# Kernel optimization log

Hardware: AMD Instinct MI355X
Metric: run time of the kernel (lower is better)

## Reference

```python
import jax, jax.numpy as jnp
import numpy as np

EPS = 1e-8  # torch.nn.CosineSimilarity default eps


def setup_inputs() -> dict:
    key = jax.random.key(0)
    k1, k2, k3 = jax.random.split(key, 3)
    B, T, D, L = 16, 256, 512, 32
    v1 = jax.random.normal(k1, (B, T, D), dtype=jnp.float32)
    v1_mask = jnp.ones((B, T), dtype=jnp.float32)
    v2 = jax.random.normal(k2, (B, D), dtype=jnp.float32)
    w = jax.random.normal(k3, (L, D), dtype=jnp.float32)
    return {"v1": v1, "v1_mask": v1_mask, "v2": v2, "w": w}


def reference(v1, v1_mask, v2, w):
    # v1: [B,T,D], v1_mask: [B,T], v2: [B,D], w: [L,D]
    # Original math: cos over D of (w * v1) and (w * v2), per perspective l.
    # Fused: (w_l*a)\cdot(w_l*b) = sum_d w[l,d]^2 a[d] b[d]; likewise for norms.
    v1m = v1 * v1_mask[:, :, None]              # [B,T,D]
    w2 = w * w                                   # [L,D]
    num = jnp.einsum('btd,ld,bd->btl', v1m, w2, v2)          # [B,T,L]
    n1 = jnp.sqrt(jnp.einsum('btd,ld->btl', v1m * v1m, w2))  # [B,T,L]
    n2 = jnp.sqrt(jnp.einsum('bd,ld->bl', v2 * v2, w2))      # [B,L]
    denom = jnp.maximum(n1 * n2[:, None, :], EPS)
    return num / denom                           # [B,T,L]
```

## Files before the change

kernel.cpp:

```cpp
#include <hip/hip_runtime.h>
#include <cstddef>

#define EPSV 1e-8f

__device__ __forceinline__ float rdlane(float x, int s) {
    return __int_as_float(__builtin_amdgcn_readlane(__float_as_int(x), s));
}

#define GLD16(gp, lp) \
    __builtin_amdgcn_global_load_lds((const __attribute__((address_space(1))) void*)(gp), \
                                     (__attribute__((address_space(3))) void*)(lp), 16, 0, 0)

__global__ __launch_bounds__(256, 2) void fullmatch_kernel(
    const float* __restrict__ v1,
    const float* __restrict__ v1_mask,
    const float* __restrict__ v2,
    const float* __restrict__ w,
    float* __restrict__ out)
{
    const int tid  = threadIdx.x;
    const int lane = tid & 63;
    const int wv   = tid >> 6;
    const int lp2  = wv & 1;
    const int dh   = wv >> 1;
    const int dh16 = __builtin_amdgcn_readfirstlane(dh) * 16;

    const int bid  = blockIdx.x;
    const int tile = bid & 63;
    const int lpg  = bid >> 6;
    const int b    = tile >> 2;
    const int t0   = (tile & 3) * 64;
    const int p    = lpg * 2 + lp2;
    const int t    = t0 + lane;

    __shared__ float v1s[2][64][128];
    __shared__ float cmb[4][64][4];

    const size_t v1base = (size_t)(b * 256 + t0) * 512;

    #pragma unroll
    for (int j = 0; j < 8; ++j) {
        const int r0 = wv * 16 + j * 2;
        const int r  = r0 + (lane >> 5);
        const int c4 = (lane & 31) ^ (r & 31);
        GLD16(v1 + v1base + (size_t)r * 512 + c4 * 4, &v1s[0][r0][0]);
    }

    float4 w2A[2], w2B[2], hA[2], hB[2];
    float n2pA = 0.f, n2pB = 0.f;
    {
        const float* __restrict__ v2b = v2 + (size_t)b * 512;
        const float* __restrict__ wAp = w + (size_t)p * 512;
        const float* __restrict__ wBp = w + (size_t)(p + 16) * 512;
        #pragma unroll
        for (int q = 0; q < 2; ++q) {
            const int k4 = q * 64 + lane;
            const float4 wa = *(const float4*)(wAp + k4 * 4);
            const float4 wb = *(const float4*)(wBp + k4 * 4);
            const float4 vv = *(const float4*)(v2b + k4 * 4);
            float4 sa, sb, ha, hb;
            sa.x = wa.x*wa.x; sa.y = wa.y*wa.y; sa.z = wa.z*wa.z; sa.w = wa.w*wa.w;
            sb.x = wb.x*wb.x; sb.y = wb.y*wb.y; sb.z = wb.z*wb.z; sb.w = wb.w*wb.w;
            ha.x = sa.x*vv.x; ha.y = sa.y*vv.y; ha.z = sa.z*vv.z; ha.w = sa.w*vv.w;
            hb.x = sb.x*vv.x; hb.y = sb.y*vv.y; hb.z = sb.z*vv.z; hb.w = sb.w*vv.w;
            w2A[q] = sa; w2B[q] = sb; hA[q] = ha; hB[q] = hb;
            n2pA += ha.x*vv.x + ha.y*vv.y + ha.z*vv.z + ha.w*vv.w;
            n2pB += hb.x*vv.x + hb.y*vv.y + hb.z*vv.z + hb.w*vv.w;
        }
    }
    #pragma unroll
    for (int m = 32; m >= 1; m >>= 1) {
        n2pA += __shfl_xor(n2pA, m, 64);
        n2pB += __shfl_xor(n2pB, m, 64);
    }

    float accNA = 0.f, accNB = 0.f, accDA = 0.f, accDB = 0.f;
    const int lm = lane & 31;

    #pragma unroll
    for (int c = 0; c < 4; ++c) {
        __syncthreads();
        if (c < 3) {
            #pragma unroll
            for (int j = 0; j < 8; ++j) {
                const int r0 = wv * 16 + j * 2;
                const int r  = r0 + (lane >> 5);
                const int c4 = (lane & 31) ^ (r & 31);
                GLD16(v1 + v1base + (size_t)r * 512 + (c + 1) * 128 + c4 * 4,
                      &v1s[(c + 1) & 1][r0][0]);
            }
        }
        const float* __restrict__ row = &v1s[c & 1][lane][0];
        #pragma unroll
        for (int j = 0; j < 16; ++j) {
            const int s  = dh16 + j;
            const float4 a = *(const float4*)(row + ((s ^ lm) << 2));
            const int li = ((c & 1) << 5) + s;
            const int q  = c >> 1;

            const float wax = rdlane(w2A[q].x, li);
            const float way = rdlane(w2A[q].y, li);
            const float waz = rdlane(w2A[q].z, li);
            const float waw = rdlane(w2A[q].w, li);
            const float wbx = rdlane(w2B[q].x, li);
            const float wby = rdlane(w2B[q].y, li);
            const float wbz = rdlane(w2B[q].z, li);
            const float wbw = rdlane(w2B[q].w, li);
            const float hax = rdlane(hA[q].x, li);
            const float hay = rdlane(hA[q].y, li);
            const float haz = rdlane(hA[q].z, li);
            const float haw = rdlane(hA[q].w, li);
            const float hbx = rdlane(hB[q].x, li);
            const float hby = rdlane(hB[q].y, li);
            const float hbz = rdlane(hB[q].z, li);
            const float hbw = rdlane(hB[q].w, li);

            const float x2 = a.x * a.x, y2 = a.y * a.y;
            const float z2 = a.z * a.z, q2 = a.w * a.w;

            accNA = fmaf(a.x, hax, accNA);
            accNA = fmaf(a.y, hay, accNA);
            accNA = fmaf(a.z, haz, accNA);
            accNA = fmaf(a.w, haw, accNA);
            accNB = fmaf(a.x, hbx, accNB);
            accNB = fmaf(a.y, hby, accNB);
            accNB = fmaf(a.z, hbz, accNB);
            accNB = fmaf(a.w, hbw, accNB);
            accDA = fmaf(x2, wax, accDA);
            accDA = fmaf(y2, way, accDA);
            accDA = fmaf(z2, waz, accDA);
            accDA = fmaf(q2, waw, accDA);
            accDB = fmaf(x2, wbx, accDB);
            accDB = fmaf(y2, wby, accDB);
            accDB = fmaf(z2, wbz, accDB);
            accDB = fmaf(q2, wbw, accDB);
        }
    }

    cmb[wv][lane][0] = accNA;
    cmb[wv][lane][1] = accNB;
    cmb[wv][lane][2] = accDA;
    cmb[wv][lane][3] = accDB;
    __syncthreads();

    if (wv < 2) {
        const float4 o = *(const float4*)(&cmb[wv + 2][lane][0]);
        const float nA = accNA + o.x;
        const float nB = accNB + o.y;
        const float dA = accDA + o.z;
        const float dB = accDB + o.w;

        const float mk  = v1_mask[b * 256 + t];
        const float amk = fabsf(mk);
        const float n2vA = sqrtf(n2pA);
        const float n2vB = sqrtf(n2pB);
        const float denA = fmaxf(sqrtf(dA) * amk * n2vA, EPSV);
        const float denB = fmaxf(sqrtf(dB) * amk * n2vB, EPSV);
        const size_t oix = (size_t)(b * 256 + t) * 32;
        out[oix + p]      = (nA * mk) / denA;
        out[oix + p + 16] = (nB * mk) / denB;
    }
}

extern "C" void kernel_launch(void* const* d_in, const int* in_sizes, int n_in,
                              void* d_out, int out_size, void* d_ws, size_t ws_size,
                              hipStream_t stream) {
    const float* v1      = (const float*)d_in[0];
    const float* v1_mask = (const float*)d_in[1];
    const float* v2      = (const float*)d_in[2];
    const float* w       = (const float*)d_in[3];
    float* out           = (float*)d_out;

    fullmatch_kernel<<<dim3(512), dim3(256), 0, stream>>>(v1, v1_mask, v2, w, out);
}
```

Measured before the change: 19.66 us.

## Split D across four waves with per-wave LDS staging and no block barriers

```diff
diff --git a/kernel.cpp b/kernel.cpp
--- a/kernel.cpp
+++ b/kernel.cpp
@@ -11,7 +11,7 @@
     __builtin_amdgcn_global_load_lds((const __attribute__((address_space(1))) void*)(gp), \
                                      (__attribute__((address_space(3))) void*)(lp), 16, 0, 0)
 
-__global__ __launch_bounds__(256, 2) void fullmatch_kernel(
+__global__ __launch_bounds__(256, 4) void fullmatch_kernel(
     const float* __restrict__ v1,
     const float* __restrict__ v1_mask,
     const float* __restrict__ v2,
@@ -21,99 +21,112 @@
     const int tid  = threadIdx.x;
     const int lane = tid & 63;
     const int wv   = tid >> 6;
-    const int lp2  = wv & 1;
-    const int dh   = wv >> 1;
-    const int dh16 = __builtin_amdgcn_readfirstlane(dh) * 16;
+    const int wvu  = __builtin_amdgcn_readfirstlane(wv);
 
     const int bid  = blockIdx.x;
     const int tile = bid & 63;
     const int lpg  = bid >> 6;
     const int b    = tile >> 2;
     const int t0   = (tile & 3) * 64;
-    const int p    = lpg * 2 + lp2;
+    const int p    = lpg;
     const int t    = t0 + lane;
 
-    __shared__ float v1s[2][64][128];
+    __shared__ float buf[4][2][64][16];
     __shared__ float cmb[4][64][4];
 
-    const size_t v1base = (size_t)(b * 256 + t0) * 512;
+    const size_t rowbase = (size_t)(b * 256 + t0) * 512;
+    const int    qoff    = wvu * 128;
 
-    #pragma unroll
-    for (int j = 0; j < 8; ++j) {
-        const int r0 = wv * 16 + j * 2;
-        const int r  = r0 + (lane >> 5);
-        const int c4 = (lane & 31) ^ (r & 31);
-        GLD16(v1 + v1base + (size_t)r * 512 + c4 * 4, &v1s[0][r0][0]);
-    }
+    #define STAGE(sc, bs)                                                          \
+        do {                                                                       \
+            _Pragma("unroll")                                                      \
+            for (int i = 0; i < 4; ++i) {                                          \
+                const int r = i * 16 + (lane >> 2);                                \
+                const int m = (lane & 3) ^ ((lane >> 3) & 3);                      \
+                GLD16(v1 + rowbase + (size_t)r * 512 + qoff + (sc) * 16 + m * 4,   \
+                      &buf[wv][bs][i * 16][0]);                                    \
+            }                                                                      \
+        } while (0)
 
-    float4 w2A[2], w2B[2], hA[2], hB[2];
+    STAGE(0, 0);
+
+    float4 w2A0, w2A1, w2B0, w2B1, hA0, hA1, hB0, hB1;
     float n2pA = 0.f, n2pB = 0.f;
     {
         const float* __restrict__ v2b = v2 + (size_t)b * 512;
         const float* __restrict__ wAp = w + (size_t)p * 512;
         const float* __restrict__ wBp = w + (size_t)(p + 16) * 512;
-        #pragma unroll
-        for (int q = 0; q < 2; ++q) {
-            const int k4 = q * 64 + lane;
-            const float4 wa = *(const float4*)(wAp + k4 * 4);
-            const float4 wb = *(const float4*)(wBp + k4 * 4);
-            const float4 vv = *(const float4*)(v2b + k4 * 4);
-            float4 sa, sb, ha, hb;
-            sa.x = wa.x*wa.x; sa.y = wa.y*wa.y; sa.z = wa.z*wa.z; sa.w = wa.w*wa.w;
-            sb.x = wb.x*wb.x; sb.y = wb.y*wb.y; sb.z = wb.z*wb.z; sb.w = wb.w*wb.w;
-            ha.x = sa.x*vv.x; ha.y = sa.y*vv.y; ha.z = sa.z*vv.z; ha.w = sa.w*vv.w;
-            hb.x = sb.x*vv.x; hb.y = sb.y*vv.y; hb.z = sb.z*vv.z; hb.w = sb.w*vv.w;
-            w2A[q] = sa; w2B[q] = sb; hA[q] = ha; hB[q] = hb;
-            n2pA += ha.x*vv.x + ha.y*vv.y + ha.z*vv.z + ha.w*vv.w;
-            n2pB += hb.x*vv.x + hb.y*vv.y + hb.z*vv.z + hb.w*vv.w;
+        {
+            const float4 wa = *(const float4*)(wAp + lane * 4);
+            const float4 wb = *(const float4*)(wBp + lane * 4);
+            const float4 vv = *(const float4*)(v2b + lane * 4);
+            w2A0.x = wa.x*wa.x; w2A0.y = wa.y*wa.y; w2A0.z = wa.z*wa.z; w2A0.w = wa.w*wa.w;
+            w2B0.x = wb.x*wb.x; w2B0.y = wb.y*wb.y; w2B0.z = wb.z*wb.z; w2B0.w = wb.w*wb.w;
+            hA0.x = w2A0.x*vv.x; hA0.y = w2A0.y*vv.y; hA0.z = w2A0.z*vv.z; hA0.w = w2A0.w*vv.w;
+            hB0.x = w2B0.x*vv.x; hB0.y = w2B0.y*vv.y; hB0.z = w2B0.z*vv.z; hB0.w = w2B0.w*vv.w;
+            n2pA += hA0.x*vv.x + hA0.y*vv.y + hA0.z*vv.z + hA0.w*vv.w;
+            n2pB += hB0.x*vv.x + hB0.y*vv.y + hB0.z*vv.z + hB0.w*vv.w;
+        }
+        {
+            const float4 wa = *(const float4*)(wAp + 256 + lane * 4);
+            const float4 wb = *(const float4*)(wBp + 256 + lane * 4);
+            const float4 vv = *(const float4*)(v2b + 256 + lane * 4);
+            w2A1.x = wa.x*wa.x; w2A1.y = wa.y*wa.y; w2A1.z = wa.z*wa.z; w2A1.w = wa.w*wa.w;
+            w2B1.x = wb.x*wb.x; w2B1.y = wb.y*wb.y; w2B1.z = wb.z*wb.z; w2B1.w = wb.w*wb.w;
+            hA1.x = w2A1.x*vv.x; hA1.y = w2A1.y*vv.y; hA1.z = w2A1.z*vv.z; hA1.w = w2A1.w*vv.w;
+            hB1.x = w2B1.x*vv.x; hB1.y = w2B1.y*vv.y; hB1.z = w2B1.z*vv.z; hB1.w = w2B1.w*vv.w;
+            n2pA += hA1.x*vv.x + hA1.y*vv.y + hA1.z*vv.z + hA1.w*vv.w;
+            n2pB += hB1.x*vv.x + hB1.y*vv.y + hB1.z*vv.z + hB1.w*vv.w;
         }
     }
-    #pragma unroll
-    for (int m = 32; m >= 1; m >>= 1) {
-        n2pA += __shfl_xor(n2pA, m, 64);
-        n2pB += __shfl_xor(n2pB, m, 64);
+    if (wvu == 0) {
+        #pragma unroll
+        for (int m = 32; m >= 1; m >>= 1) {
+            n2pA += __shfl_xor(n2pA, m, 64);
+            n2pB += __shfl_xor(n2pB, m, 64);
+        }
     }
 
+    const int hi = wvu >> 1;
+    const float4 sw2A = hi ? w2A1 : w2A0;
+    const float4 sw2B = hi ? w2B1 : w2B0;
+    const float4 shA  = hi ? hA1  : hA0;
+    const float4 shB  = hi ? hB1  : hB0;
+    const int libase  = (wvu & 1) << 5;
+
     float accNA = 0.f, accNB = 0.f, accDA = 0.f, accDB = 0.f;
-    const int lm = lane & 31;
+    const int swz = (lane >> 1) & 3;
 
-    #pragma unroll
-    for (int c = 0; c < 4; ++c) {
-        __syncthreads();
-        if (c < 3) {
-            #pragma unroll
-            for (int j = 0; j < 8; ++j) {
-                const int r0 = wv * 16 + j * 2;
-                const int r  = r0 + (lane >> 5);
-                const int c4 = (lane & 31) ^ (r & 31);
-                GLD16(v1 + v1base + (size_t)r * 512 + (c + 1) * 128 + c4 * 4,
-                      &v1s[(c + 1) & 1][r0][0]);
-            }
+    #pragma unroll 2
+    for (int sc = 0; sc < 8; ++sc) {
+        if (sc < 7) {
+            STAGE(sc + 1, (sc + 1) & 1);
+            asm volatile("s_waitcnt vmcnt(4)" ::: "memory");
+        } else {
+            asm volatile("s_waitcnt vmcnt(0)" ::: "memory");
         }
-        const float* __restrict__ row = &v1s[c & 1][lane][0];
+        const float* __restrict__ rowp = &buf[wv][sc & 1][lane][0];
         #pragma unroll
-        for (int j = 0; j < 16; ++j) {
-            const int s  = dh16 + j;
-            const float4 a = *(const float4*)(row + ((s ^ lm) << 2));
-            const int li = ((c & 1) << 5) + s;
-            const int q  = c >> 1;
+        for (int j = 0; j < 4; ++j) {
+            const float4 a = *(const float4*)(rowp + ((j ^ swz) << 2));
+            const int li = libase + sc * 4 + j;
 
-            const float wax = rdlane(w2A[q].x, li);
-            const float way = rdlane(w2A[q].y, li);
-            const float waz = rdlane(w2A[q].z, li);
-            const float waw = rdlane(w2A[q].w, li);
-            const float wbx = rdlane(w2B[q].x, li);
-            const float wby = rdlane(w2B[q].y, li);
-            const float wbz = rdlane(w2B[q].z, li);
-            const float wbw = rdlane(w2B[q].w, li);
-            const float hax = rdlane(hA[q].x, li);
-            const float hay = rdlane(hA[q].y, li);
-            const float haz = rdlane(hA[q].z, li);
-            const float haw = rdlane(hA[q].w, li);
-            const float hbx = rdlane(hB[q].x, li);
-            const float hby = rdlane(hB[q].y, li);
-            const float hbz = rdlane(hB[q].z, li);
-            const float hbw = rdlane(hB[q].w, li);
+            const float wax = rdlane(sw2A.x, li);
+            const float way = rdlane(sw2A.y, li);
+            const float waz = rdlane(sw2A.z, li);
+            const float waw = rdlane(sw2A.w, li);
+            const float wbx = rdlane(sw2B.x, li);
+            const float wby = rdlane(sw2B.y, li);
+            const float wbz = rdlane(sw2B.z, li);
+            const float wbw = rdlane(sw2B.w, li);
+            const float hax = rdlane(shA.x, li);
+            const float hay = rdlane(shA.y, li);
+            const float haz = rdlane(shA.z, li);
+            const float haw = rdlane(shA.w, li);
+            const float hbx = rdlane(shB.x, li);
+            const float hby = rdlane(shB.y, li);
+            const float hbz = rdlane(shB.z, li);
+            const float hbw = rdlane(shB.w, li);
 
             const float x2 = a.x * a.x, y2 = a.y * a.y;
             const float z2 = a.z * a.z, q2 = a.w * a.w;
@@ -143,15 +156,15 @@
     cmb[wv][lane][3] = accDB;
     __syncthreads();
 
-    if (wv < 2) {
-        const float4 o = *(const float4*)(&cmb[wv + 2][lane][0]);
-        const float nA = accNA + o.x;
-        const float nB = accNB + o.y;
-        const float dA = accDA + o.z;
-        const float dB = accDB + o.w;
-
-        const float mk  = v1_mask[b * 256 + t];
-        const float amk = fabsf(mk);
+    if (wvu == 0) {
+        float nA = accNA, nB = accNB, dA = accDA, dB = accDB;
+        #pragma unroll
+        for (int q = 1; q < 4; ++q) {
+            const float4 o = *(const float4*)(&cmb[q][lane][0]);
+            nA += o.x; nB += o.y; dA += o.z; dB += o.w;
+        }
+        const float mk   = v1_mask[b * 256 + t];
+        const float amk  = fabsf(mk);
         const float n2vA = sqrtf(n2pA);
         const float n2vB = sqrtf(n2pB);
         const float denA = fmaxf(sqrtf(dA) * amk * n2vA, EPSV);
@@ -160,6 +173,7 @@
         out[oix + p]      = (nA * mk) / denA;
         out[oix + p + 16] = (nB * mk) / denB;
     }
+    #undef STAGE
 }
 
 extern "C" void kernel_launch(void* const* d_in, const int* in_sizes, int n_in,
@@ -171,5 +185,5 @@
     const float* w       = (const float*)d_in[3];
     float* out           = (float*)d_out;
 
-    fullmatch_kernel<<<dim3(512), dim3(256), 0, stream>>>(v1, v1_mask, v2, w, out);
+    fullmatch_kernel<<<dim3(1024), dim3(256), 0, stream>>>(v1, v1_mask, v2, w, out);
 }
```

Measured after the change: 20.45 us. 1.04x slower.
